# Performance work log

Measured on AMD Instinct MI355X. Metric: run time of the kernel, lower is better.

## Reference

```python
import jax, jax.numpy as jnp
import numpy as np

BATCH = 16384
INPUT_DIM = 1024
DEGREE = 8  # selected_degree == max_degree


def setup_inputs() -> dict:
    key = jax.random.key(0)
    k1, k2 = jax.random.split(key, 2)
    x = jax.random.normal(k1, (BATCH, INPUT_DIM), dtype=jnp.float32)
    coefficients = jax.random.normal(k2, (INPUT_DIM * (DEGREE + 1),), dtype=jnp.float32) * 0.05
    horizontal_weight = jnp.ones((1,), dtype=jnp.float32)
    return {
        "x": x,
        "coefficients": coefficients,
        "horizontal_weight": horizontal_weight,
        "degree": DEGREE,
    }


def _cheb_features(x, degree):
    # x: [B, D] already in [-1, 1]; returns [B, D*(degree+1)] with layout
    # [dim0_T0..dim0_TD, dim1_T0..dim1_TD, ...] matching the torch cat order.
    Ts = [jnp.ones_like(x), x]
    for _ in range(2, degree + 1):
        Ts.append(2.0 * x * Ts[-1] - Ts[-2])  # Chebyshev T recurrence
    cheb = jnp.stack(Ts[: degree + 1], axis=-1)  # [B, D, degree+1]
    return cheb.reshape(x.shape[0], -1)


def reference(x, coefficients, horizontal_weight, degree):
    xt = jnp.tanh(x)
    X = _cheb_features(xt, degree)            # [B, D*(degree+1)]
    return horizontal_weight * (X @ coefficients)  # [B]
```

## Files before the change

### kernel.cpp

```cpp
#include <hip/hip_runtime.h>

#define THREADS 256
#define ROWS_PER_BLOCK 8
#define NBLOCKS 2048
#define DIMS 1024
#define NC 9

__device__ __forceinline__ float fast_tanh(float v) {
    float e2x = __expf(v + v);
    return 1.0f - 2.0f * __builtin_amdgcn_rcpf(e2x + 1.0f);
}

__device__ __forceinline__ float cheb_dot(float t, const float* c) {
    float t2  = t + t;
    float tm2 = 1.0f;
    float tm1 = t;
    float s = fmaf(c[1], t, c[0]);
#pragma unroll
    for (int k = 2; k <= 8; ++k) {
        float tk = fmaf(t2, tm1, -tm2);
        s = fmaf(c[k], tk, s);
        tm2 = tm1;
        tm1 = tk;
    }
    return s;
}

__global__ __launch_bounds__(THREADS, 4)
void kan_kernel(const float* __restrict__ x,
                const float* __restrict__ coef,
                const float* __restrict__ hw,
                float* __restrict__ out)
{
    const int tid  = threadIdx.x;
    const int lane = tid & 63;
    const int wave = tid >> 6;
    const int d0   = tid * 4;

    float c[4 * NC];
    {
        const float4* cp = (const float4*)(coef + (size_t)d0 * NC);
#pragma unroll
        for (int i = 0; i < 9; ++i) {
            float4 v = cp[i];
            c[i * 4 + 0] = v.x;
            c[i * 4 + 1] = v.y;
            c[i * 4 + 2] = v.z;
            c[i * 4 + 3] = v.w;
        }
    }

    __shared__ float part[4][ROWS_PER_BLOCK];
    float acc[ROWS_PER_BLOCK];

    const int row0 = blockIdx.x * ROWS_PER_BLOCK;

#pragma unroll
    for (int r = 0; r < ROWS_PER_BLOCK; ++r) {
        const float4 xv = *(const float4*)(x + (size_t)(row0 + r) * DIMS + d0);
        float s = cheb_dot(fast_tanh(xv.x), c + 0)
                + cheb_dot(fast_tanh(xv.y), c + 9)
                + cheb_dot(fast_tanh(xv.z), c + 18)
                + cheb_dot(fast_tanh(xv.w), c + 27);
#pragma unroll
        for (int off = 32; off >= 1; off >>= 1)
            s += __shfl_xor(s, off, 64);
        acc[r] = s;
    }

    if (lane == 0) {
#pragma unroll
        for (int r = 0; r < ROWS_PER_BLOCK; ++r)
            part[wave][r] = acc[r];
    }
    __syncthreads();

    if (tid < ROWS_PER_BLOCK) {
        float v = part[0][tid] + part[1][tid] + part[2][tid] + part[3][tid];
        out[row0 + tid] = hw[0] * v;
    }
}

extern "C" void kernel_launch(void* const* d_in, const int* in_sizes, int n_in,
                              void* d_out, int out_size, void* d_ws, size_t ws_size,
                              hipStream_t stream) {
    const float* x    = (const float*)d_in[0];
    const float* coef = (const float*)d_in[1];
    const float* hw   = (const float*)d_in[2];
    float* out = (float*)d_out;
    kan_kernel<<<NBLOCKS, THREADS, 0, stream>>>(x, coef, hw, out);
}
```

Before: 100.0 us.

## Convert Chebyshev coefficients to monomial basis and evaluate with Horner

Coefficients are converted once per thread from the Chebyshev basis to power-series coefficients, so each element is evaluated with 8 FMAs by Horner's rule instead of the two-FMA-per-step recurrence. All eight x rows are loaded up front so the loads can overlap, and the shuffle reductions are interleaved across four rows at a time to expose more instruction-level parallelism. The monomial form can lose some accuracy because its coefficients are large (up to 128x), and holding eight float4 rows plus 36 coefficients raises register pressure.

```diff
diff --git a/kernel.cpp b/kernel.cpp
--- a/kernel.cpp
+++ b/kernel.cpp
@@ -4,26 +4,17 @@
 #define ROWS_PER_BLOCK 8
 #define NBLOCKS 2048
 #define DIMS 1024
-#define NC 9
 
 __device__ __forceinline__ float fast_tanh(float v) {
     float e2x = __expf(v + v);
     return 1.0f - 2.0f * __builtin_amdgcn_rcpf(e2x + 1.0f);
 }
 
-__device__ __forceinline__ float cheb_dot(float t, const float* c) {
-    float t2  = t + t;
-    float tm2 = 1.0f;
-    float tm1 = t;
-    float s = fmaf(c[1], t, c[0]);
+__device__ __forceinline__ float horner9(float t, const float* a) {
+    float p = a[8];
 #pragma unroll
-    for (int k = 2; k <= 8; ++k) {
-        float tk = fmaf(t2, tm1, -tm2);
-        s = fmaf(c[k], tk, s);
-        tm2 = tm1;
-        tm1 = tk;
-    }
-    return s;
+    for (int j = 7; j >= 0; --j) p = fmaf(p, t, a[j]);
+    return p;
 }
 
 __global__ __launch_bounds__(THREADS, 4)
@@ -37,41 +28,62 @@
     const int wave = tid >> 6;
     const int d0   = tid * 4;
 
-    float c[4 * NC];
+    float a[4][9];
     {
-        const float4* cp = (const float4*)(coef + (size_t)d0 * NC);
+        float c[36];
+        const float4* cp = (const float4*)(coef + (size_t)d0 * 9);
 #pragma unroll
         for (int i = 0; i < 9; ++i) {
             float4 v = cp[i];
-            c[i * 4 + 0] = v.x;
-            c[i * 4 + 1] = v.y;
-            c[i * 4 + 2] = v.z;
-            c[i * 4 + 3] = v.w;
+            c[4 * i + 0] = v.x; c[4 * i + 1] = v.y;
+            c[4 * i + 2] = v.z; c[4 * i + 3] = v.w;
+        }
+#pragma unroll
+        for (int d = 0; d < 4; ++d) {
+            const float* cd = c + 9 * d;
+            a[d][0] = ((cd[0] - cd[2]) + (cd[4] - cd[6])) + cd[8];
+            a[d][1] = fmaf(-3.f,  cd[3], fmaf(5.f,   cd[5], fmaf(-7.f,  cd[7], cd[1])));
+            a[d][2] = fmaf(2.f,   cd[2], fmaf(-8.f,  cd[4], fmaf(18.f,  cd[6], -32.f * cd[8])));
+            a[d][3] = fmaf(4.f,   cd[3], fmaf(-20.f, cd[5], 56.f  * cd[7]));
+            a[d][4] = fmaf(8.f,   cd[4], fmaf(-48.f, cd[6], 160.f * cd[8]));
+            a[d][5] = fmaf(16.f,  cd[5], -112.f * cd[7]);
+            a[d][6] = fmaf(32.f,  cd[6], -256.f * cd[8]);
+            a[d][7] = 64.f  * cd[7];
+            a[d][8] = 128.f * cd[8];
         }
     }
 
-    __shared__ float part[4][ROWS_PER_BLOCK];
-    float acc[ROWS_PER_BLOCK];
-
     const int row0 = blockIdx.x * ROWS_PER_BLOCK;
 
+    float4 xv[ROWS_PER_BLOCK];
 #pragma unroll
-    for (int r = 0; r < ROWS_PER_BLOCK; ++r) {
-        const float4 xv = *(const float4*)(x + (size_t)(row0 + r) * DIMS + d0);
-        float s = cheb_dot(fast_tanh(xv.x), c + 0)
-                + cheb_dot(fast_tanh(xv.y), c + 9)
-                + cheb_dot(fast_tanh(xv.z), c + 18)
-                + cheb_dot(fast_tanh(xv.w), c + 27);
+    for (int r = 0; r < ROWS_PER_BLOCK; ++r)
+        xv[r] = *(const float4*)(x + (size_t)(row0 + r) * DIMS + d0);
+
+    __shared__ float part[4][ROWS_PER_BLOCK];
+
 #pragma unroll
-        for (int off = 32; off >= 1; off >>= 1)
-            s += __shfl_xor(s, off, 64);
-        acc[r] = s;
-    }
-
-    if (lane == 0) {
+    for (int g = 0; g < 2; ++g) {
+        float s[4];
 #pragma unroll
-        for (int r = 0; r < ROWS_PER_BLOCK; ++r)
-            part[wave][r] = acc[r];
+        for (int r = 0; r < 4; ++r) {
+            const float4 v = xv[g * 4 + r];
+            s[r] = horner9(fast_tanh(v.x), a[0])
+                 + horner9(fast_tanh(v.y), a[1])
+                 + horner9(fast_tanh(v.z), a[2])
+                 + horner9(fast_tanh(v.w), a[3]);
+        }
+#pragma unroll
+        for (int off = 32; off >= 1; off >>= 1) {
+#pragma unroll
+            for (int r = 0; r < 4; ++r)
+                s[r] += __shfl_xor(s[r], off, 64);
+        }
+        if (lane == 0) {
+#pragma unroll
+            for (int r = 0; r < 4; ++r)
+                part[wave][g * 4 + r] = s[r];
+        }
     }
     __syncthreads();
 
```

New measurement: 96.47 us. -3.5%, faster.
